# Kernel tuning notes

Measured on AMD Instinct MI355X. Metric: run time of the kernel, lower is better.

## Reference

```python
import jax, jax.numpy as jnp
import numpy as np

# graph/batch constants
B, N_PER, DEG, FEAT, K = 64, 1024, 16, 64, 10
N = B * N_PER            # 65536 total nodes
E = N * DEG              # 1048576 edges
HID = 2 * FEAT           # 128


def setup_inputs() -> dict:
    key = jax.random.key(0)
    ks = jax.random.split(key, 10)
    x = jax.random.normal(ks[0], (N, FEAT), jnp.float32)
    # intra-graph edges: local indices in [0, n) offset by graph id * n
    offs = (jnp.arange(B, dtype=jnp.int32) * N_PER)[:, None]
    edge_src = (jax.random.randint(ks[1], (B, N_PER * DEG), 0, N_PER, jnp.int32) + offs).reshape(-1)
    edge_dst = (jax.random.randint(ks[2], (B, N_PER * DEG), 0, N_PER, jnp.int32) + offs).reshape(-1)
    uniforms = jax.random.uniform(ks[3], (N, 3 * K), jnp.float32, 1e-6, 1.0 - 1e-6)

    def lin(k, i, o):
        s = 1.0 / np.sqrt(i)
        return jax.random.uniform(k, (i, o), jnp.float32, -s, s)

    return {
        "x": x, "edge_src": edge_src, "edge_dst": edge_dst, "uniforms": uniforms,
        "W0": lin(ks[4], FEAT, HID), "b0": jnp.zeros((HID,), jnp.float32),
        "W1": lin(ks[5], HID, HID), "b1": jnp.zeros((HID,), jnp.float32),
        "Wf": lin(ks[6], HID, HID), "bf": jnp.zeros((HID,), jnp.float32),
        "W2": lin(ks[7], 2 * HID, HID), "b2": jnp.zeros((HID,), jnp.float32),
        "W3": lin(ks[8], HID, 1), "b3": jnp.zeros((1,), jnp.float32),
    }


def _gcn_norm(src, dst):
    # GCNConv: add self-loops, symmetric deg^{-1/2} normalization
    loop = jnp.arange(N, dtype=src.dtype)
    s = jnp.concatenate([src, loop])
    d = jnp.concatenate([dst, loop])
    deg = jnp.zeros((N,), jnp.float32).at[d].add(1.0)
    dinv = jax.lax.rsqrt(deg)  # deg >= 1 because of self-loops
    return s, d, dinv[s] * dinv[d]


def _gcn(h, W, b, s, d, norm):
    h = h @ W                                                   # [N, out]
    agg = jnp.zeros((N, W.shape[1]), h.dtype).at[d].add(h[s] * norm[:, None])
    return agg + b


def reference(x, edge_src, edge_dst, uniforms, W0, b0, W1, b1, Wf, bf, W2, b2, W3, b3):
    s, d, norm = _gcn_norm(edge_src, edge_dst)
    # conv0 + global max pool + fc1 -> per-graph global info
    h0 = jax.nn.relu(_gcn(x, W0, b0, s, d, norm))               # [N, HID]
    glob = jnp.max(h0.reshape(B, N_PER, HID), axis=1) @ Wf + bf  # [B, HID]
    # two applications of the SAME conv1 (as in the source)
    h = jax.nn.relu(_gcn(h0, W1, b1, s, d, norm))
    h = jax.nn.relu(_gcn(h, W1, b1, s, d, norm))
    # ConcatenateLayer: [local, tiled global] per node (dropout is eval identity)
    h = jnp.concatenate([h, jnp.repeat(glob, N_PER, axis=0)], axis=-1)  # [N, 2*HID]
    h = jax.nn.relu(_gcn(h, W2, b2, s, d, norm))
    logits = _gcn(h, W3, b3, s, d, norm).reshape(B, N_PER)      # [B, n]
    # SampleConcrete (eval): per-graph top-k threshold mask
    th = jax.lax.top_k(logits, K)[0][:, -1]                     # kth-largest per graph
    mask = (logits >= th[:, None]).astype(jnp.float32)
    return mask.reshape(N, 1)
```

## Files before the change

### kernel.cpp

```cpp
#include <hip/hip_runtime.h>
#include <math.h>

#define NB    64
#define NPER  1024
#define NTOT  65536
#define ETOT  1048576
#define FEAT  64
#define HID   128
#define KSEL  10
#define MAXDEG 64


typedef __attribute__((ext_vector_type(8))) short bf16x8;
typedef __attribute__((ext_vector_type(4))) float f32x4;

static __device__ __forceinline__ unsigned short f2bf(float x) {
    unsigned u = __float_as_uint(x);
    return (unsigned short)((u + 0x7FFFu + ((u >> 16) & 1u)) >> 16);
}
static __device__ __forceinline__ float bf2f(unsigned short s) {
    return __uint_as_float(((unsigned)s) << 16);
}

__global__ __launch_bounds__(256) void csr_k(const int* __restrict__ src,
                                             const int* __restrict__ dst,
                                             int* __restrict__ cnt,
                                             unsigned short* __restrict__ col16) {
    int e = blockIdx.x * 256 + threadIdx.x;
    if (e >= ETOT) return;
    int d = dst[e];
    int s = src[e];
    int pos = atomicAdd(&cnt[d], 1);
    col16[(size_t)pos * NTOT + d] = (unsigned short)(s & (NPER - 1));
}

__global__ __launch_bounds__(256) void pack_k(const float* __restrict__ W0,
                                              const float* __restrict__ W1,
                                              const float* __restrict__ W2,
                                              unsigned short* __restrict__ Wph,
                                              unsigned short* __restrict__ Wpl,
                                              float* __restrict__ part) {
    if (blockIdx.x == 0) {
        for (int i = threadIdx.x; i < NB * 128; i += 256) part[i] = 0.f;
    }
    int t = blockIdx.x * 256 + threadIdx.x;
    if (t >= 320 * 128) return;
    int k = t >> 7;
    int c = t & 127;
    float v;
    size_t mb;
    int kk;
    if (k < 64)       { kk = k;       v = W0[kk * 128 + c]; mb = 0; }
    else if (k < 192) { kk = k - 64;  v = W1[kk * 128 + c]; mb = (size_t)64 * 128; }
    else              { kk = k - 192; v = W2[kk * 128 + c]; mb = (size_t)192 * 128; }
    unsigned short h  = f2bf(v);
    unsigned short lo = f2bf(v - bf2f(h));
    size_t d = mb + ((size_t)(kk >> 3) * 128 + c) * 8 + (kk & 7);
    Wph[d] = h;
    Wpl[d] = lo;
}

__global__ __launch_bounds__(1024) void agg_k(const float* __restrict__ Z,
                                              const float* __restrict__ x,
                                              const unsigned short* __restrict__ col16,
                                              const int* __restrict__ cnt,
                                              unsigned short* __restrict__ Ah,
                                              unsigned short* __restrict__ Al,
                                              int cshift,
                                              float* __restrict__ fvec) {
    __shared__ float4 sy4[4096];
    int t = threadIdx.x;
    int g = blockIdx.x >> cshift;
    int c = blockIdx.x & ((1 << cshift) - 1);
    int gbase = g << 10;

    if (x) {
#pragma unroll
        for (int j = 0; j < 4; ++j) {
            int fl = j * 1024 + t;
            int v = fl >> 2, q = fl & 3;
            float dvv = rsqrtf((float)cnt[gbase + v] + 1.0f);
            float4 z = *(const float4*)&x[(size_t)(gbase + v) * FEAT + c * 16 + q * 4];
            z.x *= dvv; z.y *= dvv; z.z *= dvv; z.w *= dvv;
            sy4[fl] = z;
        }
    } else {
        const float4* Zg4 = (const float4*)(Z + ((size_t)c * NTOT + gbase) * 16);
#pragma unroll
        for (int j = 0; j < 4; ++j) sy4[j * 1024 + t] = Zg4[j * 1024 + t];
    }
    __syncthreads();

    int f4 = t & 3;
    int vl = t >> 2;

#pragma unroll 1
    for (int pass = 0; pass < 4; ++pass) {
        int v = pass * 256 + vl;
        int gv = gbase + v;
        int n = cnt[gv];
        float dv = rsqrtf((float)n + 1.0f);
        const unsigned short* ip = col16 + gv;
        float4 acc = sy4[v * 4 + f4];
        int i = 0;
        for (; i + 4 <= n; i += 4) {
            int a0 = ip[(size_t)(i + 0) * NTOT];
            int a1 = ip[(size_t)(i + 1) * NTOT];
            int a2 = ip[(size_t)(i + 2) * NTOT];
            int a3 = ip[(size_t)(i + 3) * NTOT];
            float4 y0 = sy4[a0 * 4 + f4];
            float4 y1 = sy4[a1 * 4 + f4];
            float4 y2 = sy4[a2 * 4 + f4];
            float4 y3 = sy4[a3 * 4 + f4];
            acc.x += (y0.x + y1.x) + (y2.x + y3.x);
            acc.y += (y0.y + y1.y) + (y2.y + y3.y);
            acc.z += (y0.z + y1.z) + (y2.z + y3.z);
            acc.w += (y0.w + y1.w) + (y2.w + y3.w);
        }
        for (; i < n; ++i) {
            float4 ya = sy4[(int)ip[(size_t)i * NTOT] * 4 + f4];
            acc.x += ya.x; acc.y += ya.y; acc.z += ya.z; acc.w += ya.w;
        }
        acc.x *= dv; acc.y *= dv; acc.z *= dv; acc.w *= dv;
        int krow = c * 16 + f4 * 4;
        size_t ba = ((size_t)(krow >> 3) * NTOT + gv) * 8 + (krow & 7);
        ushort4 h, lo;
        h.x = f2bf(acc.x); lo.x = f2bf(acc.x - bf2f(h.x));
        h.y = f2bf(acc.y); lo.y = f2bf(acc.y - bf2f(h.y));
        h.z = f2bf(acc.z); lo.z = f2bf(acc.z - bf2f(h.z));
        h.w = f2bf(acc.w); lo.w = f2bf(acc.w - bf2f(h.w));
        *(ushort4*)&Ah[ba] = h;
        *(ushort4*)&Al[ba] = lo;
    }

    if (fvec && c == 0) {
        __syncthreads();
        float* sdv = (float*)sy4;
        float dv = rsqrtf((float)cnt[gbase + t] + 1.0f);
        sdv[t] = dv;
        __syncthreads();
        int n = cnt[gbase + t];
        float acc = dv;
        const unsigned short* ip = col16 + gbase + t;
        for (int i = 0; i < n; ++i) acc += sdv[ip[(size_t)i * NTOT]];
        fvec[gbase + t] = dv * acc;
    }
}

__global__ __launch_bounds__(256, 3) void gemm_k(const unsigned short* __restrict__ Ah,
                                                 const unsigned short* __restrict__ Al,
                                                 const unsigned short* __restrict__ Wph,
                                                 const unsigned short* __restrict__ Wpl,
                                                 const float* __restrict__ bias,
                                                 float* __restrict__ outZ,
                                                 int K,
                                                 const float* __restrict__ fvec,
                                                 const float* __restrict__ gproj,
                                                 float* __restrict__ part,
                                                 const float* __restrict__ W3,
                                                 const int* __restrict__ cnt,
                                                 float* __restrict__ zout) {
    __shared__ __align__(16) unsigned short sAh[64 * 128];
    __shared__ __align__(16) unsigned short sAl[64 * 128];
    __shared__ float zred[4 * 64];

    int t = threadIdx.x;
    int row0 = blockIdx.x * 64;
    int w = t >> 6;
    int l = t & 63;
    int lr = l & 15;
    int hg = l >> 4;

    f32x4 acc[4][2];
#pragma unroll
    for (int m = 0; m < 4; ++m)
#pragma unroll
        for (int n = 0; n < 2; ++n) acc[m][n] = (f32x4){0.f, 0.f, 0.f, 0.f};

    int nu = (K >> 3) << 6 >> 8;
    for (int i = 0; i < nu; ++i) {
        int u = t + i * 256;
        int p = u >> 6, r = u & 63;
        size_t src = ((size_t)p * NTOT + row0 + r) * 8;
        *(uint4*)&sAh[u * 8] = *(const uint4*)&Ah[src];
        *(uint4*)&sAl[u * 8] = *(const uint4*)&Al[src];
    }
    __syncthreads();

    int nk = K >> 5;
#pragma unroll 1
    for (int s = 0; s < nk; ++s) {
        int pb = s * 4 + hg;
        bf16x8 ah[4], al[4], bh[2], bl[2];
#pragma unroll
        for (int m = 0; m < 4; ++m) {
            ah[m] = *(const bf16x8*)&sAh[(pb * 64 + m * 16 + lr) * 8];
            al[m] = *(const bf16x8*)&sAl[(pb * 64 + m * 16 + lr) * 8];
        }
#pragma unroll
        for (int n = 0; n < 2; ++n) {
            size_t wb = ((size_t)pb * 128 + w * 32 + n * 16 + lr) * 8;
            bh[n] = *(const bf16x8*)&Wph[wb];
            bl[n] = *(const bf16x8*)&Wpl[wb];
        }
#pragma unroll
        for (int m = 0; m < 4; ++m)
#pragma unroll
            for (int n = 0; n < 2; ++n) {
                acc[m][n] = __builtin_amdgcn_mfma_f32_16x16x32_bf16(ah[m], bh[n], acc[m][n], 0, 0, 0);
                acc[m][n] = __builtin_amdgcn_mfma_f32_16x16x32_bf16(al[m], bh[n], acc[m][n], 0, 0, 0);
                acc[m][n] = __builtin_amdgcn_mfma_f32_16x16x32_bf16(ah[m], bl[n], acc[m][n], 0, 0, 0);
            }
    }

    int g = row0 >> 10;
    int wc0 = w * 32;
    float bb[2], gp[2], w3c[2];
#pragma unroll
    for (int n = 0; n < 2; ++n) {
        int col = wc0 + n * 16 + lr;
        bb[n]  = bias[col];
        gp[n]  = fvec ? gproj[(size_t)g * 128 + col] : 0.f;
        w3c[n] = zout ? W3[col] : 0.f;
    }
    float fr[4][4];
    if (fvec) {
#pragma unroll
        for (int m = 0; m < 4; ++m)
#pragma unroll
            for (int r = 0; r < 4; ++r) fr[m][r] = fvec[row0 + m * 16 + hg * 4 + r];
    }
    float dvs[4][4];
    if (outZ) {
#pragma unroll
        for (int m = 0; m < 4; ++m)
#pragma unroll
            for (int r = 0; r < 4; ++r)
                dvs[m][r] = rsqrtf((float)cnt[row0 + m * 16 + hg * 4 + r] + 1.0f);
    }
    float zp[4][4];
#pragma unroll
    for (int m = 0; m < 4; ++m)
#pragma unroll
        for (int r = 0; r < 4; ++r) zp[m][r] = 0.f;
    float cmx[2] = {0.f, 0.f};

#pragma unroll
    for (int m = 0; m < 4; ++m)
#pragma unroll
        for (int n = 0; n < 2; ++n)
#pragma unroll
            for (int r = 0; r < 4; ++r) {
                float v = acc[m][n][r] + bb[n];
                if (fvec) v += fr[m][r] * gp[n];
                v = fmaxf(v, 0.f);
                if (part) cmx[n] = fmaxf(cmx[n], v);
                if (zout) zp[m][r] += v * w3c[n];
                if (outZ) {
                    int row = row0 + m * 16 + hg * 4 + r;
                    int cidx = w * 2 + n;
                    outZ[((size_t)cidx * NTOT + row) * 16 + lr] = v * dvs[m][r];
                }
            }

    if (part) {
#pragma unroll
        for (int n = 0; n < 2; ++n) {
            float v = cmx[n];
            v = fmaxf(v, __shfl_xor(v, 16));
            v = fmaxf(v, __shfl_xor(v, 32));
            if (hg == 0)
                atomicMax((int*)&part[(size_t)g * 128 + wc0 + n * 16 + lr],
                          __float_as_int(v));
        }
    }

    if (zout) {
#pragma unroll
        for (int m = 0; m < 4; ++m)
#pragma unroll
            for (int r = 0; r < 4; ++r) {
                float v = zp[m][r];
                v += __shfl_xor(v, 1);
                v += __shfl_xor(v, 2);
                v += __shfl_xor(v, 4);
                v += __shfl_xor(v, 8);
                zp[m][r] = v;
            }
        if (lr == 0) {
#pragma unroll
            for (int m = 0; m < 4; ++m)
#pragma unroll
                for (int r = 0; r < 4; ++r)
                    zred[w * 64 + m * 16 + hg * 4 + r] = zp[m][r];
        }
        __syncthreads();
        if (t < 64) {
            float sZ = zred[t] + zred[64 + t] + zred[128 + t] + zred[192 + t];
            zout[row0 + t] = sZ * rsqrtf((float)cnt[row0 + t] + 1.0f);
        }
    }
}

__global__ __launch_bounds__(128) void glob_k(const float* __restrict__ part,
                                              const float* __restrict__ Wf,
                                              const float* __restrict__ bf,
                                              const float* __restrict__ W2,
                                              float* __restrict__ gproj) {
    __shared__ float mp[128];
    __shared__ float gl[128];
    int g = blockIdx.x, t = threadIdx.x;
    mp[t] = part[(size_t)g * 128 + t];
    __syncthreads();
    float acc = bf[t];
    for (int k = 0; k < 128; ++k) acc += mp[k] * Wf[(size_t)k * 128 + t];
    gl[t] = acc;
    __syncthreads();
    float acc2 = 0.f;
    for (int k = 0; k < 128; ++k) acc2 += gl[k] * W2[(size_t)(128 + k) * 128 + t];
    gproj[(size_t)g * 128 + t] = acc2;
}

__global__ __launch_bounds__(256) void smask_k(const float* __restrict__ z,
                                               const unsigned short* __restrict__ col16,
                                               const int* __restrict__ cnt,
                                               const float* __restrict__ b3,
                                               float* __restrict__ out) {
    __shared__ float sz[1024];
    __shared__ float sl[1024];
    __shared__ float slo[1024];
    __shared__ float rv[4];
    __shared__ int   ri[4];
    __shared__ float sth;
    int g = blockIdx.x, t = threadIdx.x;
    int wv = t >> 6, ln = t & 63;
    int base = g << 10;
#pragma unroll
    for (int i = 0; i < 4; ++i) sz[t + 256 * i] = z[base + t + 256 * i];
    __syncthreads();
    float bb = b3[0];
#pragma unroll 1
    for (int i = 0; i < 4; ++i) {
        int v = t + 256 * i;
        int gv = base + v;
        int n = cnt[gv];
        float dv = rsqrtf((float)n + 1.0f);
        float acc = sz[v];
        const unsigned short* ip = col16 + gv;
        int j = 0;
        for (; j + 2 <= n; j += 2)
            acc += sz[ip[(size_t)j * NTOT]] + sz[ip[(size_t)(j + 1) * NTOT]];
        for (; j < n; ++j) acc += sz[ip[(size_t)j * NTOT]];
        float lg = acc * dv + bb;
        sl[v] = lg; slo[v] = lg;
    }
    __syncthreads();
    for (int pass = 0; pass < KSEL; ++pass) {
        float bv = -INFINITY;
        int bi = 0;
#pragma unroll
        for (int i = 0; i < 4; ++i) {
            float v = sl[t + 256 * i];
            if (v > bv) { bv = v; bi = t + 256 * i; }
        }
#pragma unroll
        for (int off = 32; off; off >>= 1) {
            float ov = __shfl_xor(bv, off);
            int   oi = __shfl_xor(bi, off);
            if (ov > bv || (ov == bv && oi < bi)) { bv = ov; bi = oi; }
        }
        if (ln == 0) { rv[wv] = bv; ri[wv] = bi; }
        __syncthreads();
        if (t == 0) {
            float mv = rv[0]; int mi = ri[0];
#pragma unroll
            for (int q = 1; q < 4; ++q)
                if (rv[q] > mv || (rv[q] == mv && ri[q] < mi)) { mv = rv[q]; mi = ri[q]; }
            sth = mv; sl[mi] = -INFINITY;
        }
        __syncthreads();
    }
    float th = sth;
#pragma unroll
    for (int i = 0; i < 4; ++i) {
        int v = t + 256 * i;
        out[base + v] = (slo[v] >= th) ? 1.f : 0.f;
    }
}

extern "C" void kernel_launch(void* const* d_in, const int* in_sizes, int n_in,
                              void* d_out, int out_size, void* d_ws, size_t ws_size,
                              hipStream_t stream) {
    const float* x        = (const float*)d_in[0];
    const int*   edge_src = (const int*)d_in[1];
    const int*   edge_dst = (const int*)d_in[2];
    const float* W0 = (const float*)d_in[4];
    const float* b0 = (const float*)d_in[5];
    const float* W1 = (const float*)d_in[6];
    const float* b1 = (const float*)d_in[7];
    const float* Wf = (const float*)d_in[8];
    const float* bf = (const float*)d_in[9];
    const float* W2 = (const float*)d_in[10];
    const float* b2 = (const float*)d_in[11];
    const float* W3 = (const float*)d_in[12];
    const float* b3 = (const float*)d_in[13];
    float* out = (float*)d_out;

    char* w = (char*)d_ws;
    int*            cnt   = (int*)w;            w += (size_t)NTOT * 4;
    unsigned short* col16 = (unsigned short*)w; w += (size_t)NTOT * MAXDEG * 2;
    float*          fvec  = (float*)w;          w += (size_t)NTOT * 4;
    unsigned short* Ah    = (unsigned short*)w; w += (size_t)NTOT * 128 * 2;
    unsigned short* Al    = (unsigned short*)w; w += (size_t)NTOT * 128 * 2;
    float*          Q     = (float*)w;          w += (size_t)NTOT * 128 * 4;
    float*          part  = (float*)w;          w += (size_t)NB * 128 * 4;
    float*          gproj = (float*)w;          w += (size_t)NB * 128 * 4;
    float*          z     = (float*)w;          w += (size_t)NTOT * 4;
    unsigned short* Wph   = (unsigned short*)w; w += (size_t)320 * 128 * 2;
    unsigned short* Wpl   = (unsigned short*)w; w += (size_t)320 * 128 * 2;

    hipMemsetAsync(cnt, 0, (size_t)NTOT * 4, stream);
    csr_k<<<ETOT / 256, 256, 0, stream>>>(edge_src, edge_dst, cnt, col16);
    pack_k<<<160, 256, 0, stream>>>(W0, W1, W2, Wph, Wpl, part);

    agg_k<<<NB * 4, 1024, 0, stream>>>(nullptr, x, col16, cnt, Ah, Al, 2, nullptr);
    gemm_k<<<NTOT / 64, 256, 0, stream>>>(Ah, Al, Wph, Wpl, b0, Q, FEAT,
                                          nullptr, nullptr, part, nullptr, cnt, nullptr);

    glob_k<<<NB, 128, 0, stream>>>(part, Wf, bf, W2, gproj);

    agg_k<<<NB * 8, 1024, 0, stream>>>(Q, nullptr, col16, cnt, Ah, Al, 3, nullptr);
    gemm_k<<<NTOT / 64, 256, 0, stream>>>(Ah, Al, Wph + 64 * 128, Wpl + 64 * 128, b1, Q,
                                          HID, nullptr, nullptr, nullptr, nullptr, cnt,
                                          nullptr);
    agg_k<<<NB * 8, 1024, 0, stream>>>(Q, nullptr, col16, cnt, Ah, Al, 3, nullptr);
    gemm_k<<<NTOT / 64, 256, 0, stream>>>(Ah, Al, Wph + 64 * 128, Wpl + 64 * 128, b1, Q,
                                          HID, nullptr, nullptr, nullptr, nullptr, cnt,
                                          nullptr);

    agg_k<<<NB * 8, 1024, 0, stream>>>(Q, nullptr, col16, cnt, Ah, Al, 3, fvec);
    gemm_k<<<NTOT / 64, 256, 0, stream>>>(Ah, Al, Wph + 192 * 128, Wpl + 192 * 128, b2,
                                          nullptr, HID, fvec, gproj, nullptr, W3, cnt, z);

    smask_k<<<NB, 256, 0, stream>>>(z, col16, cnt, b3, out);
}
```

Baseline: 310.2 us.

## Fold memset into pack kernel, fuse glob into agg, widen smask, raise gemm occupancy

Replaces the hipMemsetAsync of the degree counts with zeroing inside pack_k, now launched before the CSR build. Removes the separate glob_k launch by appending NB extra blocks to the first conv1 aggregation; those blocks compute the global projection in parallel over 1024 threads. Rewrites smask_k to use 1024 threads per graph so each thread handles one node instead of four. Raises gemm_k's launch-bounds occupancy hint from 3 to 4 blocks, which may force register spills.

```diff
diff --git a/kernel.cpp b/kernel.cpp
--- a/kernel.cpp
+++ b/kernel.cpp
@@ -39,11 +39,13 @@
                                               const float* __restrict__ W2,
                                               unsigned short* __restrict__ Wph,
                                               unsigned short* __restrict__ Wpl,
-                                              float* __restrict__ part) {
+                                              float* __restrict__ part,
+                                              int* __restrict__ cnt) {
+    int t = blockIdx.x * 256 + threadIdx.x;
+    for (int i = t; i < NTOT; i += 160 * 256) cnt[i] = 0;
     if (blockIdx.x == 0) {
         for (int i = threadIdx.x; i < NB * 128; i += 256) part[i] = 0.f;
     }
-    int t = blockIdx.x * 256 + threadIdx.x;
     if (t >= 320 * 128) return;
     int k = t >> 7;
     int c = t & 127;
@@ -67,9 +69,50 @@
                                               unsigned short* __restrict__ Ah,
                                               unsigned short* __restrict__ Al,
                                               int cshift,
-                                              float* __restrict__ fvec) {
+                                              float* __restrict__ fvec,
+                                              const float* __restrict__ Wf,
+                                              const float* __restrict__ bfv,
+                                              const float* __restrict__ W2g,
+                                              float* __restrict__ gproj,
+                                              const float* __restrict__ part) {
     __shared__ float4 sy4[4096];
     int t = threadIdx.x;
+
+    if (Wf && (int)blockIdx.x >= (int)gridDim.x - NB) {
+        float* sm = (float*)sy4;
+        float* mp = sm;
+        float* ps = sm + 128;
+        float* gl = sm + 128 + 1024;
+        int gg = blockIdx.x - (gridDim.x - NB);
+        int o = t & 127, s8 = t >> 7;
+        if (t < 128) mp[t] = part[(size_t)gg * 128 + t];
+        __syncthreads();
+        float p = 0.f;
+#pragma unroll
+        for (int q = 0; q < 16; ++q) { int k = s8 * 16 + q; p += mp[k] * Wf[(size_t)k * 128 + o]; }
+        ps[t] = p;
+        __syncthreads();
+        if (t < 128) {
+            float a = bfv[t];
+#pragma unroll
+            for (int q = 0; q < 8; ++q) a += ps[q * 128 + t];
+            gl[t] = a;
+        }
+        __syncthreads();
+        p = 0.f;
+#pragma unroll
+        for (int q = 0; q < 16; ++q) { int k = s8 * 16 + q; p += gl[k] * W2g[(size_t)(128 + k) * 128 + o]; }
+        ps[t] = p;
+        __syncthreads();
+        if (t < 128) {
+            float a = 0.f;
+#pragma unroll
+            for (int q = 0; q < 8; ++q) a += ps[q * 128 + t];
+            gproj[(size_t)gg * 128 + t] = a;
+        }
+        return;
+    }
+
     int g = blockIdx.x >> cshift;
     int c = blockIdx.x & ((1 << cshift) - 1);
     int gbase = g << 10;
@@ -147,7 +190,7 @@
     }
 }
 
-__global__ __launch_bounds__(256, 3) void gemm_k(const unsigned short* __restrict__ Ah,
+__global__ __launch_bounds__(256, 4) void gemm_k(const unsigned short* __restrict__ Ah,
                                                  const unsigned short* __restrict__ Al,
                                                  const unsigned short* __restrict__ Wph,
                                                  const unsigned short* __restrict__ Wpl,
@@ -302,67 +345,40 @@
     }
 }
 
-__global__ __launch_bounds__(128) void glob_k(const float* __restrict__ part,
-                                              const float* __restrict__ Wf,
-                                              const float* __restrict__ bf,
-                                              const float* __restrict__ W2,
-                                              float* __restrict__ gproj) {
-    __shared__ float mp[128];
-    __shared__ float gl[128];
-    int g = blockIdx.x, t = threadIdx.x;
-    mp[t] = part[(size_t)g * 128 + t];
-    __syncthreads();
-    float acc = bf[t];
-    for (int k = 0; k < 128; ++k) acc += mp[k] * Wf[(size_t)k * 128 + t];
-    gl[t] = acc;
-    __syncthreads();
-    float acc2 = 0.f;
-    for (int k = 0; k < 128; ++k) acc2 += gl[k] * W2[(size_t)(128 + k) * 128 + t];
-    gproj[(size_t)g * 128 + t] = acc2;
-}
-
-__global__ __launch_bounds__(256) void smask_k(const float* __restrict__ z,
-                                               const unsigned short* __restrict__ col16,
-                                               const int* __restrict__ cnt,
-                                               const float* __restrict__ b3,
-                                               float* __restrict__ out) {
+__global__ __launch_bounds__(1024) void smask_k(const float* __restrict__ z,
+                                                const unsigned short* __restrict__ col16,
+                                                const int* __restrict__ cnt,
+                                                const float* __restrict__ b3,
+                                                float* __restrict__ out) {
     __shared__ float sz[1024];
     __shared__ float sl[1024];
     __shared__ float slo[1024];
-    __shared__ float rv[4];
-    __shared__ int   ri[4];
+    __shared__ float rv[16];
+    __shared__ int   ri[16];
     __shared__ float sth;
     int g = blockIdx.x, t = threadIdx.x;
     int wv = t >> 6, ln = t & 63;
     int base = g << 10;
-#pragma unroll
-    for (int i = 0; i < 4; ++i) sz[t + 256 * i] = z[base + t + 256 * i];
+    sz[t] = z[base + t];
     __syncthreads();
     float bb = b3[0];
-#pragma unroll 1
-    for (int i = 0; i < 4; ++i) {
-        int v = t + 256 * i;
-        int gv = base + v;
+    {
+        int gv = base + t;
         int n = cnt[gv];
         float dv = rsqrtf((float)n + 1.0f);
-        float acc = sz[v];
+        float acc = sz[t];
         const unsigned short* ip = col16 + gv;
         int j = 0;
         for (; j + 2 <= n; j += 2)
             acc += sz[ip[(size_t)j * NTOT]] + sz[ip[(size_t)(j + 1) * NTOT]];
         for (; j < n; ++j) acc += sz[ip[(size_t)j * NTOT]];
         float lg = acc * dv + bb;
-        sl[v] = lg; slo[v] = lg;
+        sl[t] = lg; slo[t] = lg;
     }
     __syncthreads();
     for (int pass = 0; pass < KSEL; ++pass) {
-        float bv = -INFINITY;
-        int bi = 0;
-#pragma unroll
-        for (int i = 0; i < 4; ++i) {
-            float v = sl[t + 256 * i];
-            if (v > bv) { bv = v; bi = t + 256 * i; }
-        }
+        float bv = sl[t];
+        int bi = t;
 #pragma unroll
         for (int off = 32; off; off >>= 1) {
             float ov = __shfl_xor(bv, off);
@@ -374,18 +390,14 @@
         if (t == 0) {
             float mv = rv[0]; int mi = ri[0];
 #pragma unroll
-            for (int q = 1; q < 4; ++q)
+            for (int q = 1; q < 16; ++q)
                 if (rv[q] > mv || (rv[q] == mv && ri[q] < mi)) { mv = rv[q]; mi = ri[q]; }
             sth = mv; sl[mi] = -INFINITY;
         }
         __syncthreads();
     }
     float th = sth;
-#pragma unroll
-    for (int i = 0; i < 4; ++i) {
-        int v = t + 256 * i;
-        out[base + v] = (slo[v] >= th) ? 1.f : 0.f;
-    }
+    out[base + t] = (slo[t] >= th) ? 1.f : 0.f;
 }
 
 extern "C" void kernel_launch(void* const* d_in, const int* in_sizes, int n_in,
@@ -419,28 +431,29 @@
     unsigned short* Wph   = (unsigned short*)w; w += (size_t)320 * 128 * 2;
     unsigned short* Wpl   = (unsigned short*)w; w += (size_t)320 * 128 * 2;
 
-    hipMemsetAsync(cnt, 0, (size_t)NTOT * 4, stream);
+    pack_k<<<160, 256, 0, stream>>>(W0, W1, W2, Wph, Wpl, part, cnt);
     csr_k<<<ETOT / 256, 256, 0, stream>>>(edge_src, edge_dst, cnt, col16);
-    pack_k<<<160, 256, 0, stream>>>(W0, W1, W2, Wph, Wpl, part);
-
-    agg_k<<<NB * 4, 1024, 0, stream>>>(nullptr, x, col16, cnt, Ah, Al, 2, nullptr);
+
+    agg_k<<<NB * 4, 1024, 0, stream>>>(nullptr, x, col16, cnt, Ah, Al, 2, nullptr,
+                                       nullptr, nullptr, nullptr, nullptr, nullptr);
     gemm_k<<<NTOT / 64, 256, 0, stream>>>(Ah, Al, Wph, Wpl, b0, Q, FEAT,
                                           nullptr, nullptr, part, nullptr, cnt, nullptr);
 
-    glob_k<<<NB, 128, 0, stream>>>(part, Wf, bf, W2, gproj);
-
-    agg_k<<<NB * 8, 1024, 0, stream>>>(Q, nullptr, col16, cnt, Ah, Al, 3, nullptr);
+    agg_k<<<NB * 8 + NB, 1024, 0, stream>>>(Q, nullptr, col16, cnt, Ah, Al, 3, nullptr,
+                                            Wf, bf, W2, gproj, part);
     gemm_k<<<NTOT / 64, 256, 0, stream>>>(Ah, Al, Wph + 64 * 128, Wpl + 64 * 128, b1, Q,
                                           HID, nullptr, nullptr, nullptr, nullptr, cnt,
                                           nullptr);
-    agg_k<<<NB * 8, 1024, 0, stream>>>(Q, nullptr, col16, cnt, Ah, Al, 3, nullptr);
+    agg_k<<<NB * 8, 1024, 0, stream>>>(Q, nullptr, col16, cnt, Ah, Al, 3, nullptr,
+                                       nullptr, nullptr, nullptr, nullptr, nullptr);
     gemm_k<<<NTOT / 64, 256, 0, stream>>>(Ah, Al, Wph + 64 * 128, Wpl + 64 * 128, b1, Q,
                                           HID, nullptr, nullptr, nullptr, nullptr, cnt,
                                           nullptr);
 
-    agg_k<<<NB * 8, 1024, 0, stream>>>(Q, nullptr, col16, cnt, Ah, Al, 3, fvec);
+    agg_k<<<NB * 8, 1024, 0, stream>>>(Q, nullptr, col16, cnt, Ah, Al, 3, fvec,
+                                       nullptr, nullptr, nullptr, nullptr, nullptr);
     gemm_k<<<NTOT / 64, 256, 0, stream>>>(Ah, Al, Wph + 192 * 128, Wpl + 192 * 128, b2,
                                           nullptr, HID, fvec, gproj, nullptr, W3, cnt, z);
 
-    smask_k<<<NB, 256, 0, stream>>>(z, col16, cnt, b3, out);
-}
+    smask_k<<<NB, 1024, 0, stream>>>(z, col16, cnt, b3, out);
+}
```

Measured after the change: 308.9 us. About the same (-0.4%).
